# Performance work log

Hardware: AMD Instinct MI355X
Metric: run time of the kernel (lower is better)

## Reference

```python
import jax, jax.numpy as jnp
import numpy as np

DX, DZ, DT = 10.0, 10.0, 1.0e-3
NX, NZ = 512, 512
NSTEPS, NREC = 512, 128
DT2 = DT * DT
INV_DXDZ = 1.0 / (DX * DZ)


def setup_inputs() -> dict:
    key = jax.random.key(0)
    k1, k2, k3, k4 = jax.random.split(key, 4)
    # velocity in [1500, 2500] m/s -> CFL stable with dt=1e-3, dx=dz=10
    velocity_model = 1500.0 + 1000.0 * jax.random.uniform(k1, (NX, NZ), dtype=jnp.float32)
    source = jax.random.normal(k2, (NSTEPS,), dtype=jnp.float32)
    rec_x = jax.random.randint(k3, (NREC,), 0, NX)
    rec_z = jax.random.randint(k4, (NREC,), 0, NZ)
    return {
        "velocity_model": velocity_model,
        "source": source,
        "src_x": 256,
        "src_z": 8,
        "rec_x": rec_x,
        "rec_z": rec_z,
    }


def _laplacian(p):
    # 3x3 cross stencil with zero padding, scaled by 1/(dx*dz) -- identical to
    # F.conv2d(p, [[0,1,0],[1,-4,1],[0,1,0]]/(dx*dz), padding=1)
    pp = jnp.pad(p, 1)
    return (pp[:-2, 1:-1] + pp[2:, 1:-1] + pp[1:-1, :-2] + pp[1:-1, 2:] - 4.0 * p) * INV_DXDZ


def reference(velocity_model, source, src_x, src_z, rec_x, rec_z):
    v2_dt2 = velocity_model * velocity_model * DT2  # [nx, nz]

    def step(carry, s_t):
        p, p_old = carry
        p_new = 2.0 * p - p_old + v2_dt2 * _laplacian(p)
        p_new = p_new.at[src_x, src_z].add(s_t * DT2)
        return (p_new, p), p_new[rec_x, rec_z]  # gather all receivers at once

    p0 = jnp.zeros((NX, NZ), dtype=velocity_model.dtype)
    _, recs = jax.lax.scan(step, (p0, p0), source)  # recs: [n_steps, n_rec]
    return recs.T  # seismogram: [n_rec, n_steps]
```

## Files before the change

kernel.cpp:

```cpp
#include <hip/hip_runtime.h>


#define NXd 512
#define NZd 512
#define NSTEPSd 512
#define NRECd 128
#define DT2f 1.0e-6f
#define INVf 1.0e-2f
#define TBk 16
#define TIk 32
#define EXTk 64
#define NTILEk 16
#define PADk 16
#define PWk 544
#define LROWS 66

__device__ __forceinline__ float dpp_shr1(float x) {
    int v = __builtin_amdgcn_update_dpp(0, __builtin_bit_cast(int, x),
                                        0x138, 0xF, 0xF, false);
    return __builtin_bit_cast(float, v);
}
__device__ __forceinline__ float dpp_shl1(float x) {
    int v = __builtin_amdgcn_update_dpp(0, __builtin_bit_cast(int, x),
                                        0x130, 0xF, 0xF, false);
    return __builtin_bit_cast(float, v);
}

__global__ __launch_bounds__(256) void fdtd_init(const float* __restrict__ vel,
                                                 float2* __restrict__ PA,
                                                 float2* __restrict__ PB,
                                                 float* __restrict__ V2,
                                                 float* __restrict__ out) {
    int p = blockIdx.x * blockDim.x + threadIdx.x;
    if (p < PWk * PWk) {
        int px = p / PWk, pz = p - px * PWk;
        float v2 = 0.f;
        if (px >= PADk && px < PADk + NXd && pz >= PADk && pz < PADk + NZd) {
            float v = vel[(px - PADk) * NZd + (pz - PADk)];
            v2 = v * v * (DT2f * INVf);
        }
        PA[p] = make_float2(0.f, 0.f);
        PB[p] = make_float2(0.f, 0.f);
        V2[p] = v2;
    }
    if (p < NRECd * NSTEPSd) out[p] = 0.f;
}

__global__ __launch_bounds__(1024) void fdtd_tblock(
    const float* __restrict__ source,
    const int* __restrict__ src_x, const int* __restrict__ src_z,
    const int* __restrict__ rec_x, const int* __restrict__ rec_z,
    const float2* __restrict__ Pin, float2* __restrict__ Pout,
    const float* __restrict__ V2, float* __restrict__ out,
    int t0, int ibase)
{
    __shared__ float sb[2][LROWS * EXTk];

    const int tid = threadIdx.x;
    const int w   = tid >> 6;
    const int ez  = tid & 63;
    const int gx0 = (blockIdx.y + ibase) * TIk;
    const int gz0 = blockIdx.x * TIk;
    const int ox = gx0 - TBk, oz = gz0 - TBk;
    const int gz = oz + ez;

    const int pbase = (gx0 + 4 * w) * PWk + gz0 + ez;
    float2 co[4]; float rV2i[4];
    #pragma unroll
    for (int i = 0; i < 4; ++i) {
        co[i]   = Pin[pbase + i * PWk];
        rV2i[i] = V2[pbase + i * PWk];
    }

    const int sx = *src_x, sz = *src_z;
    {
        int dxm = max(0, max(ox - sx, sx - (ox + EXTk - 1)));
        int dzm = max(0, max(oz - sz, sz - (oz + EXTk - 1)));
        if (dxm + dzm > t0 + TBk + 1) return;
    }

    bool rOwn = false; int rIdx = 0;
    if (tid < NRECd) {
        int rx = rec_x[tid], rz = rec_z[tid];
        rOwn = (rx >= gx0 && rx < gx0 + TIk && rz >= gz0 && rz < gz0 + TIk);
        rIdx = (rx - ox + 1) * EXTk + (rz - oz);
    }

    float rCur[4], rOld[4];
    #pragma unroll
    for (int i = 0; i < 4; ++i) {
        rCur[i] = co[i].x; rOld[i] = co[i].y;
        sb[0][(4 * w + 1 + i) * EXTk + ez] = rCur[i];
    }
    if (w == 0) {
        sb[0][ez] = 0.f;
        sb[0][(LROWS - 1) * EXTk + ez] = 0.f;
        sb[1][ez] = 0.f;
        sb[1][(LROWS - 1) * EXTk + ez] = 0.f;
    }

    const int exs = sx - ox, ezs = sz - oz;
    const bool srcHere = (exs >= 0 && exs < EXTk && ezs >= 0 && ezs < EXTk) &&
                         (tid == (((exs >> 2) << 6) | ezs));
    float sv[TBk];
    if (srcHere) {
        #pragma unroll
        for (int s = 0; s < TBk; ++s) sv[s] = source[t0 + s] * DT2f;
    }

    __syncthreads();

    const int fbase = 4 * w * EXTk + ez;

    float rv[TBk];
    #pragma unroll
    for (int s = 0; s < TBk; ++s) {
        const float* cur = sb[s & 1];
        float* nxt = sb[(s & 1) ^ 1];
        const float up0 = cur[fbase];
        const float dn3 = cur[fbase + 5 * EXTk];
        float nv[4];
        #pragma unroll
        for (int i = 0; i < 4; ++i) {
            const float up = (i == 0) ? up0 : rCur[i - 1];
            const float dn = (i == 3) ? dn3 : rCur[i + 1];
            const float lf = dpp_shr1(rCur[i]);
            const float rt = dpp_shl1(rCur[i]);
            const float sum = (up + dn) + (lf + rt);
            const float t4 = __builtin_fmaf(-4.0f, rCur[i], sum);
            const float pm = __builtin_fmaf(2.0f, rCur[i], -rOld[i]);
            nv[i] = __builtin_fmaf(rV2i[i], t4, pm);
        }
        #pragma unroll
        for (int i = 0; i < 4; ++i) {
            rOld[i] = rCur[i];
            rCur[i] = nv[i];
            nxt[fbase + (1 + i) * EXTk] = nv[i];
        }
        if (srcHere) {
            #pragma unroll
            for (int i = 0; i < 4; ++i) {
                if (i == (exs & 3)) {
                    rCur[i] += sv[s];
                    nxt[(exs + 1) * EXTk + ezs] = rCur[i];
                }
            }
        }
        __syncthreads();
        if (rOwn) rv[s] = nxt[rIdx];
    }

    if (w >= 4 && w < 12 && ez >= TBk && ez < EXTk - TBk) {
        #pragma unroll
        for (int i = 0; i < 4; ++i)
            Pout[pbase + i * PWk] = make_float2(rCur[i], rOld[i]);
    }

    if (rOwn) {
        #pragma unroll
        for (int s = 0; s < TBk; ++s)
            out[tid * NSTEPSd + t0 + s] = rv[s];
    }
}

extern "C" void kernel_launch(void* const* d_in, const int* in_sizes, int n_in,
                              void* d_out, int out_size, void* d_ws, size_t ws_size,
                              hipStream_t stream) {
    const float* vel    = (const float*)d_in[0];
    const float* source = (const float*)d_in[1];
    const int*   src_x  = (const int*)d_in[2];
    const int*   src_z  = (const int*)d_in[3];
    const int*   rec_x  = (const int*)d_in[4];
    const int*   rec_z  = (const int*)d_in[5];
    float* out = (float*)d_out;

    const size_t FP = (size_t)PWk * PWk;
    float2* PA = (float2*)d_ws;
    float2* PB = PA + FP;
    float*  V2 = (float*)(PB + FP);

    fdtd_init<<<(PWk * PWk + 255) / 256, 256, 0, stream>>>(vel, PA, PB, V2, out);

    for (int k = 0; k < NSTEPSd / TBk; ++k) {
        const int R = 16 * k + TBk + 1 + 32;
        const int tneg = 209 - R;
        int ilo = tneg > 0 ? (tneg + 31) / 32 : 0;
        int ihi = (272 + R) / 32; if (ihi > 15) ihi = 15;
        int jhi = (24 + R) / 32;  if (jhi > 15) jhi = 15;

        const float2* Pin = (k & 1) ? PB : PA;
        float2* Pout      = (k & 1) ? PA : PB;
        dim3 grid(jhi + 1, ihi - ilo + 1);
        fdtd_tblock<<<grid, dim3(1024), 0, stream>>>(source, src_x, src_z,
                                                     rec_x, rec_z, Pin, Pout,
                                                     V2, out, 16 * k, ilo);
    }
}
```

Measured before the change: 361.5 us.

## Replace per-step block barrier with neighbor-wave LDS flags and register receiver reads

Each time step no longer ends with a block-wide __syncthreads. Instead every wave publishes a step counter in LDS and spins until its two neighbouring waves have reached the same step before it reads halo rows. Receiver samples are now routed at setup, through atomic exchanges, to the thread that owns that cell, so the value is taken straight from registers instead of re-reading shared memory after a barrier. This aims to cut barrier stalls and let waves drift relative to each other. In exchange it adds spin-wait polling, extra LDS for the routing tables, and a limit of three receivers per cell.

```diff
diff --git a/kernel.cpp b/kernel.cpp
--- a/kernel.cpp
+++ b/kernel.cpp
@@ -10,7 +10,6 @@
 #define TBk 16
 #define TIk 32
 #define EXTk 64
-#define NTILEk 16
 #define PADk 16
 #define PWk 544
 #define LROWS 66
@@ -24,6 +23,9 @@
     int v = __builtin_amdgcn_update_dpp(0, __builtin_bit_cast(int, x),
                                         0x130, 0xF, 0xF, false);
     return __builtin_bit_cast(float, v);
+}
+__device__ __forceinline__ float sel4(int r, float a, float b, float c, float d) {
+    return (r == 0) ? a : (r == 1) ? b : (r == 2) ? c : d;
 }
 
 __global__ __launch_bounds__(256) void fdtd_init(const float* __restrict__ vel,
@@ -55,6 +57,8 @@
     int t0, int ibase)
 {
     __shared__ float sb[2][LROWS * EXTk];
+    __shared__ int route0[1024], route1[1024], route2[1024];
+    __shared__ int wctr[16];
 
     const int tid = threadIdx.x;
     const int w   = tid >> 6;
@@ -62,7 +66,6 @@
     const int gx0 = (blockIdx.y + ibase) * TIk;
     const int gz0 = blockIdx.x * TIk;
     const int ox = gx0 - TBk, oz = gz0 - TBk;
-    const int gz = oz + ez;
 
     const int pbase = (gx0 + 4 * w) * PWk + gz0 + ez;
     float2 co[4]; float rV2i[4];
@@ -79,13 +82,8 @@
         if (dxm + dzm > t0 + TBk + 1) return;
     }
 
-    bool rOwn = false; int rIdx = 0;
-    if (tid < NRECd) {
-        int rx = rec_x[tid], rz = rec_z[tid];
-        rOwn = (rx >= gx0 && rx < gx0 + TIk && rz >= gz0 && rz < gz0 + TIk);
-        rIdx = (rx - ox + 1) * EXTk + (rz - oz);
-    }
-
+    route0[tid] = -1; route1[tid] = -1; route2[tid] = -1;
+    if (tid < 16) wctr[tid] = 0;
     float rCur[4], rOld[4];
     #pragma unroll
     for (int i = 0; i < 4; ++i) {
@@ -98,6 +96,23 @@
         sb[1][ez] = 0.f;
         sb[1][(LROWS - 1) * EXTk + ez] = 0.f;
     }
+    __syncthreads();
+
+    if (tid < NRECd) {
+        int rx = rec_x[tid], rz = rec_z[tid];
+        if (rx >= gx0 && rx < gx0 + TIk && rz >= gz0 && rz < gz0 + TIk) {
+            int f = rx - ox, c = rz - oz;
+            int owner = ((f >> 2) << 6) | c;
+            int pack = (tid << 2) | (f & 3);
+            int prev = atomicExch(&route0[owner], pack);
+            if (prev != -1) {
+                prev = atomicExch(&route1[owner], prev);
+                if (prev != -1) atomicExch(&route2[owner], prev);
+            }
+        }
+    }
+    __syncthreads();
+    const int myR0 = route0[tid], myR1 = route1[tid], myR2 = route2[tid];
 
     const int exs = sx - ox, ezs = sz - oz;
     const bool srcHere = (exs >= 0 && exs < EXTk && ezs >= 0 && ezs < EXTk) &&
@@ -108,13 +123,18 @@
         for (int s = 0; s < TBk; ++s) sv[s] = source[t0 + s] * DT2f;
     }
 
-    __syncthreads();
-
     const int fbase = 4 * w * EXTk + ez;
 
     float rv[TBk];
     #pragma unroll
     for (int s = 0; s < TBk; ++s) {
+        if (w > 0)
+            while (__hip_atomic_load(&wctr[w - 1], __ATOMIC_ACQUIRE,
+                                     __HIP_MEMORY_SCOPE_WORKGROUP) < s) {}
+        if (w < 15)
+            while (__hip_atomic_load(&wctr[w + 1], __ATOMIC_ACQUIRE,
+                                     __HIP_MEMORY_SCOPE_WORKGROUP) < s) {}
+
         const float* cur = sb[s & 1];
         float* nxt = sb[(s & 1) ^ 1];
         const float up0 = cur[fbase];
@@ -146,8 +166,14 @@
                 }
             }
         }
-        __syncthreads();
-        if (rOwn) rv[s] = nxt[rIdx];
+        if (myR0 >= 0) rv[s] = sel4(myR0 & 3, rCur[0], rCur[1], rCur[2], rCur[3]);
+        if (myR1 >= 0) out[(myR1 >> 2) * NSTEPSd + t0 + s] =
+                            sel4(myR1 & 3, rCur[0], rCur[1], rCur[2], rCur[3]);
+        if (myR2 >= 0) out[(myR2 >> 2) * NSTEPSd + t0 + s] =
+                            sel4(myR2 & 3, rCur[0], rCur[1], rCur[2], rCur[3]);
+        if (ez == 0)
+            __hip_atomic_store(&wctr[w], s + 1, __ATOMIC_RELEASE,
+                               __HIP_MEMORY_SCOPE_WORKGROUP);
     }
 
     if (w >= 4 && w < 12 && ez >= TBk && ez < EXTk - TBk) {
@@ -156,10 +182,11 @@
             Pout[pbase + i * PWk] = make_float2(rCur[i], rOld[i]);
     }
 
-    if (rOwn) {
+    if (myR0 >= 0) {
+        const int rec = myR0 >> 2;
         #pragma unroll
         for (int s = 0; s < TBk; ++s)
-            out[tid * NSTEPSd + t0 + s] = rv[s];
+            out[rec * NSTEPSd + t0 + s] = rv[s];
     }
 }
 
```

Result: slower. 382.9 us (+5.9%).

## Advance two timesteps per LDS exchange using redundant halo rows in registers

Applied to the files above, without the earlier changes.

Each thread now keeps one extra row above and below its four-row strip and computes two time steps per shared-memory exchange, which halves the number of __syncthreads and LDS round trips in the temporal-blocking loop. The padding grows to 18 and the LDS buffer to 68 rows to cover the wider halo. Receiver sampling no longer reads back from LDS after each barrier. A precomputed per-tile table, built by a new init kernel, maps each thread to up to three receivers, and the value is picked from registers. The cost is redundant stencil work on the extra rows, more register pressure, and scattered global writes when several receivers share one thread.

```diff
diff --git a/kernel.cpp b/kernel.cpp
--- a/kernel.cpp
+++ b/kernel.cpp
@@ -10,10 +10,10 @@
 #define TBk 16
 #define TIk 32
 #define EXTk 64
-#define NTILEk 16
-#define PADk 16
-#define PWk 544
-#define LROWS 66
+#define PADk 18
+#define PWk 548
+#define LROWS 68
+#define NTILES 256
 
 __device__ __forceinline__ float dpp_shr1(float x) {
     int v = __builtin_amdgcn_update_dpp(0, __builtin_bit_cast(int, x),
@@ -25,12 +25,27 @@
                                         0x130, 0xF, 0xF, false);
     return __builtin_bit_cast(float, v);
 }
-
-__global__ __launch_bounds__(256) void fdtd_init(const float* __restrict__ vel,
-                                                 float2* __restrict__ PA,
-                                                 float2* __restrict__ PB,
-                                                 float* __restrict__ V2,
-                                                 float* __restrict__ out) {
+__device__ __forceinline__ float upd(float c, float o, float v2,
+                                     float up, float dn) {
+    float lf = dpp_shr1(c);
+    float rt = dpp_shl1(c);
+    float sum = (up + dn) + (lf + rt);
+    float t4 = __builtin_fmaf(-4.0f, c, sum);
+    float pm = __builtin_fmaf(2.0f, c, -o);
+    return __builtin_fmaf(v2, t4, pm);
+}
+__device__ __forceinline__ float sel4(int r, float a, float b, float c, float d) {
+    return (r == 0) ? a : (r == 1) ? b : (r == 2) ? c : d;
+}
+
+__global__ __launch_bounds__(256) void fdtd_init1(const float* __restrict__ vel,
+                                                  float2* __restrict__ PA,
+                                                  float2* __restrict__ PB,
+                                                  float* __restrict__ V2,
+                                                  float* __restrict__ out,
+                                                  int* __restrict__ RT0,
+                                                  int* __restrict__ RT1,
+                                                  int* __restrict__ RT2) {
     int p = blockIdx.x * blockDim.x + threadIdx.x;
     if (p < PWk * PWk) {
         int px = p / PWk, pz = p - px * PWk;
@@ -44,33 +59,61 @@
         V2[p] = v2;
     }
     if (p < NRECd * NSTEPSd) out[p] = 0.f;
+    if (p < NTILES * 1024) { RT0[p] = -1; RT1[p] = -1; RT2[p] = -1; }
+}
+
+__global__ __launch_bounds__(128) void fdtd_init2(const int* __restrict__ rec_x,
+                                                  const int* __restrict__ rec_z,
+                                                  int* __restrict__ RT0,
+                                                  int* __restrict__ RT1,
+                                                  int* __restrict__ RT2) {
+    int r = threadIdx.x;
+    if (r < NRECd) {
+        int rx = rec_x[r], rz = rec_z[r];
+        int ty = rx >> 5, tz = rz >> 5;
+        int f = (rx & 31) + TBk;
+        int c = (rz & 31) + TBk;
+        int owner = ((f >> 2) << 6) | c;
+        int idx = ((ty * 16 + tz) << 10) + owner;
+        int pack = (r << 2) | (f & 3);
+        int prev = atomicExch(&RT0[idx], pack);
+        if (prev != -1) {
+            prev = atomicExch(&RT1[idx], prev);
+            if (prev != -1) atomicExch(&RT2[idx], prev);
+        }
+    }
 }
 
 __global__ __launch_bounds__(1024) void fdtd_tblock(
     const float* __restrict__ source,
     const int* __restrict__ src_x, const int* __restrict__ src_z,
-    const int* __restrict__ rec_x, const int* __restrict__ rec_z,
     const float2* __restrict__ Pin, float2* __restrict__ Pout,
     const float* __restrict__ V2, float* __restrict__ out,
-    int t0, int ibase)
+    const int* __restrict__ RT0, const int* __restrict__ RT1,
+    const int* __restrict__ RT2, int t0, int ibase)
 {
     __shared__ float sb[2][LROWS * EXTk];
 
     const int tid = threadIdx.x;
     const int w   = tid >> 6;
     const int ez  = tid & 63;
-    const int gx0 = (blockIdx.y + ibase) * TIk;
-    const int gz0 = blockIdx.x * TIk;
+    const int ty  = blockIdx.y + ibase, tz = blockIdx.x;
+    const int gx0 = ty * TIk, gz0 = tz * TIk;
     const int ox = gx0 - TBk, oz = gz0 - TBk;
-    const int gz = oz + ez;
-
-    const int pbase = (gx0 + 4 * w) * PWk + gz0 + ez;
+
+    const int pbase = (gx0 + 4 * w + 2) * PWk + gz0 + ez + 2;
     float2 co[4]; float rV2i[4];
     #pragma unroll
     for (int i = 0; i < 4; ++i) {
         co[i]   = Pin[pbase + i * PWk];
         rV2i[i] = V2[pbase + i * PWk];
     }
+    float rOldX0 = Pin[pbase - PWk].y;
+    float rOldX1 = Pin[pbase + 4 * PWk].y;
+    const float rV2X0 = V2[pbase - PWk];
+    const float rV2X1 = V2[pbase + 4 * PWk];
+    const int rtb = ((ty * 16 + tz) << 10) + tid;
+    const int m0 = RT0[rtb], m1 = RT1[rtb], m2 = RT2[rtb];
 
     const int sx = *src_x, sz = *src_z;
     {
@@ -79,75 +122,91 @@
         if (dxm + dzm > t0 + TBk + 1) return;
     }
 
-    bool rOwn = false; int rIdx = 0;
-    if (tid < NRECd) {
-        int rx = rec_x[tid], rz = rec_z[tid];
-        rOwn = (rx >= gx0 && rx < gx0 + TIk && rz >= gz0 && rz < gz0 + TIk);
-        rIdx = (rx - ox + 1) * EXTk + (rz - oz);
-    }
-
     float rCur[4], rOld[4];
     #pragma unroll
     for (int i = 0; i < 4; ++i) {
         rCur[i] = co[i].x; rOld[i] = co[i].y;
-        sb[0][(4 * w + 1 + i) * EXTk + ez] = rCur[i];
+        sb[0][(4 * w + 2 + i) * EXTk + ez] = rCur[i];
     }
     if (w == 0) {
-        sb[0][ez] = 0.f;
-        sb[0][(LROWS - 1) * EXTk + ez] = 0.f;
-        sb[1][ez] = 0.f;
-        sb[1][(LROWS - 1) * EXTk + ez] = 0.f;
+        #pragma unroll
+        for (int b = 0; b < 2; ++b) {
+            sb[b][ez] = 0.f;
+            sb[b][EXTk + ez] = 0.f;
+            sb[b][66 * EXTk + ez] = 0.f;
+            sb[b][67 * EXTk + ez] = 0.f;
+        }
     }
 
     const int exs = sx - ox, ezs = sz - oz;
-    const bool srcHere = (exs >= 0 && exs < EXTk && ezs >= 0 && ezs < EXTk) &&
-                         (tid == (((exs >> 2) << 6) | ezs));
+    const bool zok = (ezs >= 0 && ezs < EXTk) && (ez == ezs);
+    const bool srcA = zok && (exs >= 4 * w - 1) && (exs <= 4 * w + 4);
+    const bool srcB = zok && (exs >= 4 * w) && (exs <= 4 * w + 3);
     float sv[TBk];
-    if (srcHere) {
+    if (srcA) {
         #pragma unroll
         for (int s = 0; s < TBk; ++s) sv[s] = source[t0 + s] * DT2f;
     }
 
     __syncthreads();
 
-    const int fbase = 4 * w * EXTk + ez;
+    const int lbase = 4 * w * EXTk + ez;
 
     float rv[TBk];
     #pragma unroll
-    for (int s = 0; s < TBk; ++s) {
-        const float* cur = sb[s & 1];
-        float* nxt = sb[(s & 1) ^ 1];
-        const float up0 = cur[fbase];
-        const float dn3 = cur[fbase + 5 * EXTk];
-        float nv[4];
-        #pragma unroll
-        for (int i = 0; i < 4; ++i) {
-            const float up = (i == 0) ? up0 : rCur[i - 1];
-            const float dn = (i == 3) ? dn3 : rCur[i + 1];
-            const float lf = dpp_shr1(rCur[i]);
-            const float rt = dpp_shl1(rCur[i]);
-            const float sum = (up + dn) + (lf + rt);
-            const float t4 = __builtin_fmaf(-4.0f, rCur[i], sum);
-            const float pm = __builtin_fmaf(2.0f, rCur[i], -rOld[i]);
-            nv[i] = __builtin_fmaf(rV2i[i], t4, pm);
-        }
-        #pragma unroll
-        for (int i = 0; i < 4; ++i) {
-            rOld[i] = rCur[i];
-            rCur[i] = nv[i];
-            nxt[fbase + (1 + i) * EXTk] = nv[i];
-        }
-        if (srcHere) {
-            #pragma unroll
-            for (int i = 0; i < 4; ++i) {
-                if (i == (exs & 3)) {
-                    rCur[i] += sv[s];
-                    nxt[(exs + 1) * EXTk + ezs] = rCur[i];
-                }
-            }
-        }
+    for (int r = 0; r < TBk / 2; ++r) {
+        const float* cb = sb[r & 1];
+        float* nb = sb[(r & 1) ^ 1];
+        const float cm2 = cb[lbase];
+        const float cm1 = cb[lbase + EXTk];
+        const float cp1 = cb[lbase + 6 * EXTk];
+        const float cp2 = cb[lbase + 7 * EXTk];
+
+        float a0 = upd(cm1,     rOldX0,  rV2X0,   cm2,     rCur[0]);
+        float a1 = upd(rCur[0], rOld[0], rV2i[0], cm1,     rCur[1]);
+        float a2 = upd(rCur[1], rOld[1], rV2i[1], rCur[0], rCur[2]);
+        float a3 = upd(rCur[2], rOld[2], rV2i[2], rCur[1], rCur[3]);
+        float a4 = upd(rCur[3], rOld[3], rV2i[3], rCur[2], cp1);
+        float a5 = upd(cp1,     rOldX1,  rV2X1,   rCur[3], cp2);
+        if (srcA) {
+            const float svA = sv[2 * r];
+            const int d = exs - (4 * w - 1);
+            if (d == 0) a0 += svA; else if (d == 1) a1 += svA;
+            else if (d == 2) a2 += svA; else if (d == 3) a3 += svA;
+            else if (d == 4) a4 += svA; else a5 += svA;
+        }
+        if (m0 >= 0) rv[2 * r] = sel4(m0 & 3, a1, a2, a3, a4);
+        if (m1 >= 0) out[(m1 >> 2) * NSTEPSd + t0 + 2 * r] =
+                          sel4(m1 & 3, a1, a2, a3, a4);
+        if (m2 >= 0) out[(m2 >> 2) * NSTEPSd + t0 + 2 * r] =
+                          sel4(m2 & 3, a1, a2, a3, a4);
+
+        float b0 = upd(a1, rCur[0], rV2i[0], a0, a2);
+        float b1 = upd(a2, rCur[1], rV2i[1], a1, a3);
+        float b2 = upd(a3, rCur[2], rV2i[2], a2, a4);
+        float b3 = upd(a4, rCur[3], rV2i[3], a3, a5);
+        if (srcB) {
+            const float svB = sv[2 * r + 1];
+            const int i = exs - 4 * w;
+            if (i == 0) b0 += svB; else if (i == 1) b1 += svB;
+            else if (i == 2) b2 += svB; else b3 += svB;
+        }
+        if (m0 >= 0) rv[2 * r + 1] = sel4(m0 & 3, b0, b1, b2, b3);
+        if (m1 >= 0) out[(m1 >> 2) * NSTEPSd + t0 + 2 * r + 1] =
+                          sel4(m1 & 3, b0, b1, b2, b3);
+        if (m2 >= 0) out[(m2 >> 2) * NSTEPSd + t0 + 2 * r + 1] =
+                          sel4(m2 & 3, b0, b1, b2, b3);
+
+        rOld[0] = a1; rCur[0] = b0;
+        rOld[1] = a2; rCur[1] = b1;
+        rOld[2] = a3; rCur[2] = b2;
+        rOld[3] = a4; rCur[3] = b3;
+        rOldX0 = a0; rOldX1 = a5;
+        nb[lbase + 2 * EXTk] = b0;
+        nb[lbase + 3 * EXTk] = b1;
+        nb[lbase + 4 * EXTk] = b2;
+        nb[lbase + 5 * EXTk] = b3;
         __syncthreads();
-        if (rOwn) rv[s] = nxt[rIdx];
     }
 
     if (w >= 4 && w < 12 && ez >= TBk && ez < EXTk - TBk) {
@@ -156,10 +215,11 @@
             Pout[pbase + i * PWk] = make_float2(rCur[i], rOld[i]);
     }
 
-    if (rOwn) {
+    if (m0 >= 0) {
+        const int rec = m0 >> 2;
         #pragma unroll
         for (int s = 0; s < TBk; ++s)
-            out[tid * NSTEPSd + t0 + s] = rv[s];
+            out[rec * NSTEPSd + t0 + s] = rv[s];
     }
 }
 
@@ -178,8 +238,13 @@
     float2* PA = (float2*)d_ws;
     float2* PB = PA + FP;
     float*  V2 = (float*)(PB + FP);
-
-    fdtd_init<<<(PWk * PWk + 255) / 256, 256, 0, stream>>>(vel, PA, PB, V2, out);
+    int*    RT0 = (int*)(V2 + FP);
+    int*    RT1 = RT0 + NTILES * 1024;
+    int*    RT2 = RT1 + NTILES * 1024;
+
+    fdtd_init1<<<(PWk * PWk + 255) / 256, 256, 0, stream>>>(vel, PA, PB, V2,
+                                                            out, RT0, RT1, RT2);
+    fdtd_init2<<<1, 128, 0, stream>>>(rec_x, rec_z, RT0, RT1, RT2);
 
     for (int k = 0; k < NSTEPSd / TBk; ++k) {
         const int R = 16 * k + TBk + 1 + 32;
@@ -192,7 +257,8 @@
         float2* Pout      = (k & 1) ? PA : PB;
         dim3 grid(jhi + 1, ihi - ilo + 1);
         fdtd_tblock<<<grid, dim3(1024), 0, stream>>>(source, src_x, src_z,
-                                                     rec_x, rec_z, Pin, Pout,
-                                                     V2, out, 16 * k, ilo);
-    }
-}
+                                                     Pin, Pout, V2, out,
+                                                     RT0, RT1, RT2,
+                                                     16 * k, ilo);
+    }
+}
```

New measurement: 433.7 us. 20.0% more time.
